# Kernel tuning notes

Hardware: AMD Instinct MI355X
Metric: run time of the kernel (lower is better)

## Reference

```python
import jax, jax.numpy as jnp
import numpy as np

BATCH, SEQ, HID, OUT = 4, 4096, 4096, 4096
N_ADAPTERS, RANK = 8, 64
ALPHA = 1.0


def setup_inputs() -> dict:
    key = jax.random.key(0)
    k1, k2, k3, k4 = jax.random.split(key, 4)
    x = jax.random.normal(k1, (BATCH, SEQ, HID), dtype=jnp.float32)
    adapter_ids = jax.random.randint(k2, (BATCH,), 0, N_ADAPTERS, dtype=jnp.int32)
    # A: per-adapter up-projection (n_adapters, rank, out); original init randn*0.02
    A = jax.random.normal(k3, (N_ADAPTERS, RANK, OUT), dtype=jnp.float32) * 0.02
    # B: per-adapter down-projection (hid, n_adapters, rank); original init is zeros,
    # use small random values so the baseline output is non-trivial.
    B = jax.random.normal(k4, (HID, N_ADAPTERS, RANK), dtype=jnp.float32) * 0.02
    return {"x": x, "adapter_ids": adapter_ids, "A": A, "B": B}


def reference(x, adapter_ids, A, B):
    # Equivalent dense math of the stk block-sparse sdd+dsd:
    # out[b] = (x[b] @ B[:, a, :]) @ A[a] * (alpha / rank),  a = adapter_ids[b]
    n_adapters, rank, out_f = A.shape
    B_sel = jnp.take(B, adapter_ids, axis=1)       # (hid, batch, rank)
    A_sel = jnp.take(A, adapter_ids, axis=0)       # (batch, rank, out)
    Bx = jnp.einsum('bsh,hbr->bsr', x, B_sel)      # sampled-dense-dense
    out = jnp.einsum('bsr,bro->bso', Bx, A_sel)    # dense-sparse-dense
    scaling = jnp.asarray(ALPHA / rank, dtype=out.dtype)
    return out * scaling
```

## Files before the change

### kernel.cpp

```cpp
#include <hip/hip_runtime.h>

#define BATCH 4
#define SEQ   4096
#define HID   4096
#define OUTF  4096
#define NA    8
#define RANK  64

typedef __attribute__((ext_vector_type(8))) short  short8;
typedef __attribute__((ext_vector_type(4))) float  f32x4;
typedef __attribute__((ext_vector_type(2))) unsigned int u32x2;

__device__ __forceinline__ unsigned short cvt_bf16(float f) {
  return (unsigned short)((__float_as_uint(f) + 0x8000u) >> 16);
}
__device__ __forceinline__ unsigned int pack_bf16_2(float lo, float hi) {
  unsigned int a = __float_as_uint(lo);
  unsigned int b = __float_as_uint(hi);
  return ((a + 0x8000u) >> 16) | ((b + 0x8000u) & 0xFFFF0000u);
}

__global__ __launch_bounds__(256) void prep_kernel(
    const float* __restrict__ A, const float* __restrict__ Bm,
    unsigned short* __restrict__ Bct, unsigned short* __restrict__ Act) {
  __shared__ unsigned short lds[64 * 72];
  int bid = blockIdx.x;
  int t   = threadIdx.x;
  int lo  = t & 63;
  int hi4 = t >> 6;
  if (bid < 512) {
    int a  = bid >> 6;
    int h0 = (bid & 63) << 6;
    #pragma unroll
    for (int p = 0; p < 16; ++p) {
      int hl = (p << 2) + hi4;
      float v = Bm[((size_t)(h0 + hl) * NA + a) * RANK + lo];
      lds[lo * 72 + hl] = cvt_bf16(v);
    }
    __syncthreads();
    #pragma unroll
    for (int p = 0; p < 16; ++p) {
      int rl = (p << 2) + hi4;
      Bct[((size_t)a * RANK + rl) * HID + h0 + lo] = lds[rl * 72 + lo];
    }
  } else {
    int b2 = bid - 512;
    int a  = b2 >> 6;
    int o0 = (b2 & 63) << 6;
    #pragma unroll
    for (int p = 0; p < 16; ++p) {
      int rl = (p << 2) + hi4;
      float v = A[((size_t)a * RANK + rl) * OUTF + o0 + lo];
      lds[lo * 72 + rl] = cvt_bf16(v);
    }
    __syncthreads();
    #pragma unroll
    for (int p = 0; p < 16; ++p) {
      int ol = (p << 2) + hi4;
      Act[((size_t)a * OUTF + o0 + ol) * RANK + lo] = lds[ol * 72 + lo];
    }
  }
}

__global__ __launch_bounds__(512, 8) void fused_kernel(
    const float* __restrict__ x, const int* __restrict__ ids,
    const unsigned short* __restrict__ Bct, const unsigned short* __restrict__ Act,
    float* __restrict__ out) {
  __shared__ float smem[8 * 16 * 65];
  __shared__ unsigned short bx[16 * 72];
  unsigned short* xs = (unsigned short*)smem;
  float*          os = smem;
  float*          red = smem;

  int bid   = blockIdx.x;
  int batch = bid & 3;
  int s0    = (bid >> 2) << 4;
  int t     = threadIdx.x;
  int w     = t >> 6;
  int lane  = t & 63;
  int m     = lane & 15;
  int q     = lane >> 4;
  int a     = ids[batch];

  const float* xg = x + (size_t)(batch * SEQ + s0) * HID;
  const unsigned short* bbase = Bct + (size_t)a * RANK * HID;

  f32x4 acc[4];
  #pragma unroll
  for (int nt = 0; nt < 4; ++nt) acc[nt] = (f32x4){0.f, 0.f, 0.f, 0.f};

  for (int kc = 0; kc < 4; ++kc) {
    if (kc) __syncthreads();
    f32x4 v[8];
    #pragma unroll
    for (int r = 0; r < 8; ++r) {
      int flat = (r << 11) + (t << 2);
      int row  = flat >> 10;
      int col  = flat & 1023;
      v[r] = __builtin_nontemporal_load(
          (const f32x4*)(xg + (size_t)row * HID + (kc << 10) + col));
    }
    #pragma unroll
    for (int r = 0; r < 8; ++r) {
      int flat = (r << 11) + (t << 2);
      int row  = flat >> 10;
      int col  = flat & 1023;
      int csw  = (col >> 3) ^ (row & 7);
      u32x2 pk;
      pk[0] = pack_bf16_2(v[r][0], v[r][1]);
      pk[1] = pack_bf16_2(v[r][2], v[r][3]);
      *(u32x2*)&xs[row * 1024 + (csw << 3) + (col & 7)] = pk;
    }
    __syncthreads();
    #pragma unroll
    for (int j = 0; j < 4; ++j) {
      int kl  = (w << 7) + (j << 5) + (q << 3);
      int csw = (kl >> 3) ^ (m & 7);
      short8 af = *(const short8*)&xs[m * 1024 + (csw << 3)];
      int kglob = (kc << 10) + kl;
      #pragma unroll
      for (int nt = 0; nt < 4; ++nt) {
        short8 bf = *(const short8*)(bbase + (size_t)(nt * 16 + m) * HID + kglob);
        acc[nt] = __builtin_amdgcn_mfma_f32_16x16x32_bf16(af, bf, acc[nt], 0, 0, 0);
      }
    }
  }
  __syncthreads();

  #pragma unroll
  for (int nt = 0; nt < 4; ++nt)
    #pragma unroll
    for (int r = 0; r < 4; ++r)
      red[(w * 16 + q * 4 + r) * 65 + nt * 16 + m] = acc[nt][r];
  __syncthreads();

  if (t < 256) {
    int row = t >> 4;
    int rb  = (t & 15) << 2;
    float v0 = 0.f, v1 = 0.f, v2 = 0.f, v3 = 0.f;
    #pragma unroll
    for (int ww = 0; ww < 8; ++ww) {
      const float* rr = &red[(ww * 16 + row) * 65 + rb];
      v0 += rr[0]; v1 += rr[1]; v2 += rr[2]; v3 += rr[3];
    }
    const float sc = 1.0f / 64.0f;
    uint2 pk;
    pk.x = pack_bf16_2(v0 * sc, v1 * sc);
    pk.y = pack_bf16_2(v2 * sc, v3 * sc);
    *(uint2*)&bx[row * 72 + rb] = pk;
  }
  __syncthreads();

  short8 p0 = *(const short8*)&bx[m * 72 + (q << 3)];
  short8 p1 = *(const short8*)&bx[m * 72 + 32 + (q << 3)];
  const unsigned short* abase = Act + (size_t)a * OUTF * RANK;

  for (int oc = 0; oc < 8; ++oc) {
    int o0 = oc << 9;
    #pragma unroll
    for (int nt = 0; nt < 4; ++nt) {
      const unsigned short* arow =
          abase + (size_t)(o0 + (w << 6) + nt * 16 + m) * RANK;
      short8 b0 = *(const short8*)(arow + (q << 3));
      short8 b1 = *(const short8*)(arow + 32 + (q << 3));
      f32x4 cc = (f32x4){0.f, 0.f, 0.f, 0.f};
      cc = __builtin_amdgcn_mfma_f32_16x16x32_bf16(b0, p0, cc, 0, 0, 0);
      cc = __builtin_amdgcn_mfma_f32_16x16x32_bf16(b1, p1, cc, 0, 0, 0);
      int ci  = (w << 4) + (nt << 2) + q;
      *(f32x4*)&os[m * 512 + ((ci ^ (m & 7)) << 2)] = cc;
    }
    __syncthreads();
    #pragma unroll
    for (int r = 0; r < 4; ++r) {
      int flat = (r << 11) + (t << 2);
      int row  = flat >> 9;
      int col  = flat & 511;
      int csw  = (col >> 2) ^ (row & 7);
      f32x4 vv = *(const f32x4*)&os[row * 512 + (csw << 2)];
      *(f32x4*)(out + (size_t)(batch * SEQ + s0 + row) * OUTF + o0 + col) = vv;
    }
    __syncthreads();
  }
}

extern "C" void kernel_launch(void* const* d_in, const int* in_sizes, int n_in,
                              void* d_out, int out_size, void* d_ws, size_t ws_size,
                              hipStream_t stream) {
  const float* x   = (const float*)d_in[0];
  const int*   ids = (const int*)d_in[1];
  const float* A   = (const float*)d_in[2];
  const float* Bm  = (const float*)d_in[3];
  float*       out = (float*)d_out;

  unsigned short* Bct = (unsigned short*)d_ws;
  unsigned short* Act = Bct + (size_t)NA * RANK * HID;

  prep_kernel <<<1024, 256, 0, stream>>>(A, Bm, Bct, Act);
  fused_kernel<<<1024, 512, 0, stream>>>(x, ids, Bct, Act, out);
}
```

Baseline: 565.9 us.

## Prefetch next x chunk into registers and use raw barriers without vmem waits

The next 1024-column chunk of x is loaded into registers while the current chunk is converted and staged in LDS, and the loads are left in flight across the MFMA phase. Plain __syncthreads is replaced with s_barrier plus an lgkmcnt-only wait, so the barriers no longer wait on outstanding global loads or stores. The output phase computes the MFMAs for the next column chunk before the barrier, which overlaps them with the previous chunk's global stores. In exchange the launch bound drops to 4 waves per SIMD to make room for the extra live registers, and correctness now depends on the hand-placed barriers.

```diff
diff --git a/kernel.cpp b/kernel.cpp
--- a/kernel.cpp
+++ b/kernel.cpp
@@ -18,6 +18,18 @@
   unsigned int a = __float_as_uint(lo);
   unsigned int b = __float_as_uint(hi);
   return ((a + 0x8000u) >> 16) | ((b + 0x8000u) & 0xFFFF0000u);
+}
+
+__device__ __forceinline__ void raw_barrier() {
+  __builtin_amdgcn_sched_barrier(0);
+  __builtin_amdgcn_s_barrier();
+  __builtin_amdgcn_sched_barrier(0);
+}
+__device__ __forceinline__ void lds_fence_barrier() {
+  __builtin_amdgcn_sched_barrier(0);
+  asm volatile("s_waitcnt lgkmcnt(0)" ::: "memory");
+  __builtin_amdgcn_s_barrier();
+  __builtin_amdgcn_sched_barrier(0);
 }
 
 __global__ __launch_bounds__(256) void prep_kernel(
@@ -62,7 +74,7 @@
   }
 }
 
-__global__ __launch_bounds__(512, 8) void fused_kernel(
+__global__ __launch_bounds__(512, 4) void fused_kernel(
     const float* __restrict__ x, const int* __restrict__ ids,
     const unsigned short* __restrict__ Bct, const unsigned short* __restrict__ Act,
     float* __restrict__ out) {
@@ -89,17 +101,17 @@
   #pragma unroll
   for (int nt = 0; nt < 4; ++nt) acc[nt] = (f32x4){0.f, 0.f, 0.f, 0.f};
 
+  f32x4 v[8];
+  #pragma unroll
+  for (int r = 0; r < 8; ++r) {
+    int flat = (r << 11) + (t << 2);
+    v[r] = __builtin_nontemporal_load(
+        (const f32x4*)(xg + (size_t)(flat >> 10) * HID + (flat & 1023)));
+  }
+
+  #pragma unroll
   for (int kc = 0; kc < 4; ++kc) {
-    if (kc) __syncthreads();
-    f32x4 v[8];
-    #pragma unroll
-    for (int r = 0; r < 8; ++r) {
-      int flat = (r << 11) + (t << 2);
-      int row  = flat >> 10;
-      int col  = flat & 1023;
-      v[r] = __builtin_nontemporal_load(
-          (const f32x4*)(xg + (size_t)row * HID + (kc << 10) + col));
-    }
+    if (kc) raw_barrier();
     #pragma unroll
     for (int r = 0; r < 8; ++r) {
       int flat = (r << 11) + (t << 2);
@@ -111,7 +123,15 @@
       pk[1] = pack_bf16_2(v[r][2], v[r][3]);
       *(u32x2*)&xs[row * 1024 + (csw << 3) + (col & 7)] = pk;
     }
-    __syncthreads();
+    if (kc < 3) {
+      #pragma unroll
+      for (int r = 0; r < 8; ++r) {
+        int flat = (r << 11) + (t << 2);
+        v[r] = __builtin_nontemporal_load(
+            (const f32x4*)(xg + (size_t)(flat >> 10) * HID + ((kc + 1) << 10) + (flat & 1023)));
+      }
+    }
+    lds_fence_barrier();
     #pragma unroll
     for (int j = 0; j < 4; ++j) {
       int kl  = (w << 7) + (j << 5) + (q << 3);
@@ -154,22 +174,28 @@
   short8 p0 = *(const short8*)&bx[m * 72 + (q << 3)];
   short8 p1 = *(const short8*)&bx[m * 72 + 32 + (q << 3)];
   const unsigned short* abase = Act + (size_t)a * OUTF * RANK;
+  float* outp = out + (size_t)(batch * SEQ + s0) * OUTF;
 
   for (int oc = 0; oc < 8; ++oc) {
     int o0 = oc << 9;
+    f32x4 cc[4];
     #pragma unroll
     for (int nt = 0; nt < 4; ++nt) {
       const unsigned short* arow =
           abase + (size_t)(o0 + (w << 6) + nt * 16 + m) * RANK;
       short8 b0 = *(const short8*)(arow + (q << 3));
       short8 b1 = *(const short8*)(arow + 32 + (q << 3));
-      f32x4 cc = (f32x4){0.f, 0.f, 0.f, 0.f};
-      cc = __builtin_amdgcn_mfma_f32_16x16x32_bf16(b0, p0, cc, 0, 0, 0);
-      cc = __builtin_amdgcn_mfma_f32_16x16x32_bf16(b1, p1, cc, 0, 0, 0);
-      int ci  = (w << 4) + (nt << 2) + q;
-      *(f32x4*)&os[m * 512 + ((ci ^ (m & 7)) << 2)] = cc;
-    }
-    __syncthreads();
+      cc[nt] = (f32x4){0.f, 0.f, 0.f, 0.f};
+      cc[nt] = __builtin_amdgcn_mfma_f32_16x16x32_bf16(b0, p0, cc[nt], 0, 0, 0);
+      cc[nt] = __builtin_amdgcn_mfma_f32_16x16x32_bf16(b1, p1, cc[nt], 0, 0, 0);
+    }
+    if (oc) raw_barrier();
+    #pragma unroll
+    for (int nt = 0; nt < 4; ++nt) {
+      int ci = (w << 4) + (nt << 2) + q;
+      *(f32x4*)&os[m * 512 + ((ci ^ (m & 7)) << 2)] = cc[nt];
+    }
+    lds_fence_barrier();
     #pragma unroll
     for (int r = 0; r < 4; ++r) {
       int flat = (r << 11) + (t << 2);
@@ -177,9 +203,8 @@
       int col  = flat & 511;
       int csw  = (col >> 2) ^ (row & 7);
       f32x4 vv = *(const f32x4*)&os[row * 512 + (csw << 2)];
-      *(f32x4*)(out + (size_t)(batch * SEQ + s0 + row) * OUTF + o0 + col) = vv;
-    }
-    __syncthreads();
+      *(f32x4*)(outp + (size_t)row * OUTF + o0 + col) = vv;
+    }
   }
 }
 
```

New measurement: 514.2 us. 9.1% less time.
